# Kernel tuning notes

Hardware: AMD Instinct MI355X
Metric: run time of the kernel (lower is better)

Reference implementation:

```python
import jax, jax.numpy as jnp
import numpy as np

N, M, LOC_MAX, EMB, D = 16, 100, 10000, 128, 4  # batch, max_len, n_locations, emb_dim, delta feature dim


def setup_inputs() -> dict:
    key = jax.random.key(0)
    k1, k2, k3, k4, k5 = jax.random.split(key, 5)
    return {
        "self_attn": jax.random.normal(k1, (N, M, EMB), jnp.float32),
        "self_delta": jax.random.normal(k2, (N, M, LOC_MAX, D), jnp.float32),
        "traj_len": jax.random.randint(k3, (N,), 0, M),  # unused by forward (kept for signature fidelity)
        "emb_table": jax.random.normal(k4, (LOC_MAX + 1, EMB), jnp.float32) * 0.02,
        "value_w": jax.random.normal(k5, (M,), jnp.float32) * 0.1,  # Linear(max_len, 1, bias=False) weight
    }


def reference(self_attn, self_delta, traj_len, emb_table, value_w):
    # self_delta: [N, M, L, D] -> sum last dim -> [N, M, L] -> transpose -> [N, L, M]
    delta = jnp.sum(self_delta, axis=-1).transpose(0, 2, 1)
    # candidates = 1..loc_max (same for every batch row), so gather once: [L, EMB]
    emb_cand = emb_table[1:LOC_MAX + 1]
    # bmm(emb_candidates, self_attn^T) -> [N, L, M], then elementwise decay
    attn = jnp.einsum('ld,nmd->nlm', emb_cand, self_attn) * delta
    # Linear(max_len, 1, bias=False) over last axis, view to [N, L]
    return jnp.einsum('nlm,m->nl', attn, value_w)
```

## Files before the change

kernel.cpp:

```cpp
#include <hip/hip_runtime.h>

#define N_   16
#define M_   100
#define L_   10000
#define EMB_ 128
#define TL   64
#define NT   256
#define MT   112
#define BDP  136
#define DWP  68
#define NIT  25

typedef _Float16 half8   __attribute__((ext_vector_type(8)));
typedef _Float16 half4v  __attribute__((ext_vector_type(4)));
typedef float    floatx4 __attribute__((ext_vector_type(4)));

__global__ __launch_bounds__(NT, 3) void attn_fused_kernel(
    const float* __restrict__ self_attn,
    const float* __restrict__ self_delta,
    const float* __restrict__ emb_table,
    const float* __restrict__ value_w,
    float* __restrict__ out)
{
    __shared__ _Float16 B_s[MT * BDP];
    __shared__ _Float16 dw_s[MT * DWP];

    const int n   = blockIdx.y;
    const int l0  = blockIdx.x * TL;
    const int tid = threadIdx.x;

    const float4* dp = (const float4*)self_delta + (size_t)n * M_ * L_;
    float4 dv[NIT];
    #pragma unroll
    for (int it = 0; it < NIT; ++it) {
        int idx = tid + it * NT;
        int ll  = idx & (TL - 1);
        int m   = idx >> 6;
        int l   = l0 + ll;
        float4 z = {0.f, 0.f, 0.f, 0.f};
        dv[it] = (l < L_) ? dp[(size_t)m * L_ + l] : z;
    }

    for (int i = tid; i < 12 * BDP; i += NT)
        B_s[100 * BDP + i] = (_Float16)0.f;
    for (int i = tid; i < 12 * DWP; i += NT)
        dw_s[100 * DWP + i] = (_Float16)0.f;

    const float4* ap = (const float4*)(self_attn + (size_t)n * M_ * EMB_);
    for (int i = tid; i < M_ * EMB_ / 4; i += NT) {
        int m  = i >> 5;
        int d4 = (i & 31) * 4;
        float wv  = value_w[m];
        float4 av = ap[i];
        half4v h;
        h[0] = (_Float16)(av.x * wv); h[1] = (_Float16)(av.y * wv);
        h[2] = (_Float16)(av.z * wv); h[3] = (_Float16)(av.w * wv);
        *(half4v*)&B_s[m * BDP + d4] = h;
    }

    #pragma unroll
    for (int it = 0; it < NIT; ++it) {
        int idx = tid + it * NT;
        int ll  = idx & (TL - 1);
        int m   = idx >> 6;
        float4 d4 = dv[it];
        dw_s[m * DWP + ll] = (_Float16)(d4.x + d4.y + d4.z + d4.w);
    }
    __syncthreads();

    const int lane = tid & 63;
    const int wid  = tid >> 6;
    const int row  = lane & 15;
    const int q    = lane >> 4;

    floatx4 acc[7];
    #pragma unroll
    for (int t = 0; t < 7; ++t) acc[t] = (floatx4){0.f, 0.f, 0.f, 0.f};

    int al = l0 + wid * 16 + row + 1;
    if (al > L_) al = L_;
    const float* ep = emb_table + (size_t)al * EMB_ + q * 8;

    #pragma unroll
    for (int kc = 0; kc < 4; ++kc) {
        float4 e0 = *(const float4*)(ep + kc * 32);
        float4 e1 = *(const float4*)(ep + kc * 32 + 4);
        half8 a;
        a[0] = (_Float16)e0.x; a[1] = (_Float16)e0.y;
        a[2] = (_Float16)e0.z; a[3] = (_Float16)e0.w;
        a[4] = (_Float16)e1.x; a[5] = (_Float16)e1.y;
        a[6] = (_Float16)e1.z; a[7] = (_Float16)e1.w;
        const int dbase = q * 8 + kc * 32;
        #pragma unroll
        for (int t = 0; t < 7; ++t) {
            half8 b = *(const half8*)&B_s[(t * 16 + row) * BDP + dbase];
            acc[t] = __builtin_amdgcn_mfma_f32_16x16x32_f16(a, b, acc[t], 0, 0, 0);
        }
    }

    const int lbase = wid * 16 + q * 4;
    float part[4] = {0.f, 0.f, 0.f, 0.f};
    #pragma unroll
    for (int t = 0; t < 7; ++t) {
        int m = t * 16 + row;
        #pragma unroll
        for (int r = 0; r < 4; ++r) {
            float dw = (float)dw_s[m * DWP + lbase + r];
            part[r] += acc[t][r] * dw;
        }
    }
    #pragma unroll
    for (int off = 1; off < 16; off <<= 1) {
        #pragma unroll
        for (int r = 0; r < 4; ++r) part[r] += __shfl_xor(part[r], off);
    }
    if (row == 0) {
        #pragma unroll
        for (int r = 0; r < 4; ++r) {
            int l = l0 + lbase + r;
            if (l < L_) out[(size_t)n * L_ + l] = part[r];
        }
    }
}

extern "C" void kernel_launch(void* const* d_in, const int* in_sizes, int n_in,
                              void* d_out, int out_size, void* d_ws, size_t ws_size,
                              hipStream_t stream) {
    const float* self_attn  = (const float*)d_in[0];
    const float* self_delta = (const float*)d_in[1];
    const float* emb_table  = (const float*)d_in[3];
    const float* value_w    = (const float*)d_in[4];
    float* out = (float*)d_out;

    dim3 grid((L_ + TL - 1) / TL, N_);
    attn_fused_kernel<<<grid, NT, 0, stream>>>(self_attn, self_delta, emb_table, value_w, out);
}
```

Baseline: 363.0 us.

## Make blocks persistent over L tiles and prefetch next delta tile into registers

The grid shrinks to 32 blocks per batch row, and each block loops over several L tiles. B_s (attn times value weights) is built once per block and reused across its tiles. The next tile's self_delta is loaded into registers while MFMA work runs on the current tile, and those loads use nontemporal hints. The aim is to overlap the dominant delta stream with compute and amortise the B setup. The cost is fewer blocks in flight (512 total, launch bounds lowered to 2), so memory-level parallelism may be lower than with the original 2512 blocks.

```diff
diff --git a/kernel.cpp b/kernel.cpp
--- a/kernel.cpp
+++ b/kernel.cpp
@@ -1,21 +1,23 @@
 #include <hip/hip_runtime.h>
 
-#define N_   16
-#define M_   100
-#define L_   10000
-#define EMB_ 128
-#define TL   64
-#define NT   256
-#define MT   112
-#define BDP  136
-#define DWP  68
-#define NIT  25
+#define N_    16
+#define M_    100
+#define L_    10000
+#define EMB_  128
+#define TL    64
+#define NT    256
+#define MT    112
+#define BDP   136
+#define DWP   68
+#define NIT   25
+#define NTILES 157
+#define NBX   32
 
 typedef _Float16 half8   __attribute__((ext_vector_type(8)));
 typedef _Float16 half4v  __attribute__((ext_vector_type(4)));
 typedef float    floatx4 __attribute__((ext_vector_type(4)));
 
-__global__ __launch_bounds__(NT, 3) void attn_fused_kernel(
+__global__ __launch_bounds__(NT, 2) void attn_fused_kernel(
     const float* __restrict__ self_attn,
     const float* __restrict__ self_delta,
     const float* __restrict__ emb_table,
@@ -26,19 +28,23 @@
     __shared__ _Float16 dw_s[MT * DWP];
 
     const int n   = blockIdx.y;
-    const int l0  = blockIdx.x * TL;
+    const int bx  = blockIdx.x;
     const int tid = threadIdx.x;
 
-    const float4* dp = (const float4*)self_delta + (size_t)n * M_ * L_;
-    float4 dv[NIT];
-    #pragma unroll
-    for (int it = 0; it < NIT; ++it) {
-        int idx = tid + it * NT;
-        int ll  = idx & (TL - 1);
-        int m   = idx >> 6;
-        int l   = l0 + ll;
-        float4 z = {0.f, 0.f, 0.f, 0.f};
-        dv[it] = (l < L_) ? dp[(size_t)m * L_ + l] : z;
+    const floatx4* dp = (const floatx4*)self_delta + (size_t)n * M_ * L_;
+
+    floatx4 dv[NIT];
+    {
+        const int l0 = bx * TL;
+        #pragma unroll
+        for (int it = 0; it < NIT; ++it) {
+            int idx = tid + it * NT;
+            int ll  = idx & (TL - 1);
+            int m   = idx >> 6;
+            int l   = l0 + ll;
+            floatx4 z = {0.f, 0.f, 0.f, 0.f};
+            dv[it] = (l < L_) ? __builtin_nontemporal_load(&dp[(size_t)m * L_ + l]) : z;
+        }
     }
 
     for (int i = tid; i < 12 * BDP; i += NT)
@@ -58,68 +64,88 @@
         *(half4v*)&B_s[m * BDP + d4] = h;
     }
 
-    #pragma unroll
-    for (int it = 0; it < NIT; ++it) {
-        int idx = tid + it * NT;
-        int ll  = idx & (TL - 1);
-        int m   = idx >> 6;
-        float4 d4 = dv[it];
-        dw_s[m * DWP + ll] = (_Float16)(d4.x + d4.y + d4.z + d4.w);
-    }
-    __syncthreads();
+    const int lane  = tid & 63;
+    const int wid   = tid >> 6;
+    const int row   = lane & 15;
+    const int q     = lane >> 4;
+    const int lbase = wid * 16 + q * 4;
 
-    const int lane = tid & 63;
-    const int wid  = tid >> 6;
-    const int row  = lane & 15;
-    const int q    = lane >> 4;
+    for (int t = bx; t < NTILES; t += NBX) {
+        const int l0 = t * TL;
 
-    floatx4 acc[7];
-    #pragma unroll
-    for (int t = 0; t < 7; ++t) acc[t] = (floatx4){0.f, 0.f, 0.f, 0.f};
+        #pragma unroll
+        for (int it = 0; it < NIT; ++it) {
+            int idx = tid + it * NT;
+            int ll  = idx & (TL - 1);
+            int m   = idx >> 6;
+            floatx4 d4 = dv[it];
+            dw_s[m * DWP + ll] = (_Float16)(d4.x + d4.y + d4.z + d4.w);
+        }
+        __syncthreads();
 
-    int al = l0 + wid * 16 + row + 1;
-    if (al > L_) al = L_;
-    const float* ep = emb_table + (size_t)al * EMB_ + q * 8;
+        const int tn = t + NBX;
+        if (tn < NTILES) {
+            const int l0n = tn * TL;
+            #pragma unroll
+            for (int it = 0; it < NIT; ++it) {
+                int idx = tid + it * NT;
+                int ll  = idx & (TL - 1);
+                int m   = idx >> 6;
+                int l   = l0n + ll;
+                floatx4 z = {0.f, 0.f, 0.f, 0.f};
+                dv[it] = (l < L_) ? __builtin_nontemporal_load(&dp[(size_t)m * L_ + l]) : z;
+            }
+        }
 
-    #pragma unroll
-    for (int kc = 0; kc < 4; ++kc) {
-        float4 e0 = *(const float4*)(ep + kc * 32);
-        float4 e1 = *(const float4*)(ep + kc * 32 + 4);
-        half8 a;
-        a[0] = (_Float16)e0.x; a[1] = (_Float16)e0.y;
-        a[2] = (_Float16)e0.z; a[3] = (_Float16)e0.w;
-        a[4] = (_Float16)e1.x; a[5] = (_Float16)e1.y;
-        a[6] = (_Float16)e1.z; a[7] = (_Float16)e1.w;
-        const int dbase = q * 8 + kc * 32;
+        floatx4 acc[7];
         #pragma unroll
-        for (int t = 0; t < 7; ++t) {
-            half8 b = *(const half8*)&B_s[(t * 16 + row) * BDP + dbase];
-            acc[t] = __builtin_amdgcn_mfma_f32_16x16x32_f16(a, b, acc[t], 0, 0, 0);
+        for (int tt = 0; tt < 7; ++tt) acc[tt] = (floatx4){0.f, 0.f, 0.f, 0.f};
+
+        int al = l0 + wid * 16 + row + 1;
+        if (al > L_) al = L_;
+        const float* ep = emb_table + (size_t)al * EMB_ + q * 8;
+
+        #pragma unroll
+        for (int kc = 0; kc < 4; ++kc) {
+            float4 e0 = *(const float4*)(ep + kc * 32);
+            float4 e1 = *(const float4*)(ep + kc * 32 + 4);
+            half8 a;
+            a[0] = (_Float16)e0.x; a[1] = (_Float16)e0.y;
+            a[2] = (_Float16)e0.z; a[3] = (_Float16)e0.w;
+            a[4] = (_Float16)e1.x; a[5] = (_Float16)e1.y;
+            a[6] = (_Float16)e1.z; a[7] = (_Float16)e1.w;
+            const int dbase = q * 8 + kc * 32;
+            #pragma unroll
+            for (int tt = 0; tt < 7; ++tt) {
+                half8 b = *(const half8*)&B_s[(tt * 16 + row) * BDP + dbase];
+                acc[tt] = __builtin_amdgcn_mfma_f32_16x16x32_f16(a, b, acc[tt], 0, 0, 0);
+            }
         }
-    }
 
-    const int lbase = wid * 16 + q * 4;
-    float part[4] = {0.f, 0.f, 0.f, 0.f};
-    #pragma unroll
-    for (int t = 0; t < 7; ++t) {
-        int m = t * 16 + row;
+        float part[4] = {0.f, 0.f, 0.f, 0.f};
         #pragma unroll
-        for (int r = 0; r < 4; ++r) {
-            float dw = (float)dw_s[m * DWP + lbase + r];
-            part[r] += acc[t][r] * dw;
+        for (int tt = 0; tt < 7; ++tt) {
+            int m = tt * 16 + row;
+            #pragma unroll
+            for (int r = 0; r < 4; ++r) {
+                float dwv = (float)dw_s[m * DWP + lbase + r];
+                part[r] += acc[tt][r] * dwv;
+            }
         }
-    }
-    #pragma unroll
-    for (int off = 1; off < 16; off <<= 1) {
         #pragma unroll
-        for (int r = 0; r < 4; ++r) part[r] += __shfl_xor(part[r], off);
-    }
-    if (row == 0) {
-        #pragma unroll
-        for (int r = 0; r < 4; ++r) {
-            int l = l0 + lbase + r;
-            if (l < L_) out[(size_t)n * L_ + l] = part[r];
+        for (int off = 1; off < 16; off <<= 1) {
+            #pragma unroll
+            for (int r = 0; r < 4; ++r) part[r] += __shfl_xor(part[r], off);
         }
+        if (row == 0) {
+            #pragma unroll
+            for (int r = 0; r < 4; ++r) {
+                int l = l0 + lbase + r;
+                if (l < L_) out[(size_t)n * L_ + l] = part[r];
+            }
+        }
+
+        if (tn < NTILES) __syncthreads();
     }
 }
 
@@ -132,6 +158,6 @@
     const float* value_w    = (const float*)d_in[4];
     float* out = (float*)d_out;
 
-    dim3 grid((L_ + TL - 1) / TL, N_);
+    dim3 grid(NBX, N_);
     attn_fused_kernel<<<grid, NT, 0, stream>>>(self_attn, self_delta, emb_table, value_w, out);
 }
```

After: 353.8 us. 1.03x faster.
